# Kernel tuning notes

Hardware: AMD Instinct MI355X
Metric: run time of the kernel (lower is better)

Reference implementation:

```python
import math
import jax, jax.numpy as jnp
import numpy as np

B, N, DQ, DK, DV, H = 8, 1024, 256, 256, 256, 8
EPS_SM = 1e-15
EPS_LN = 1e-5


def _layer_norm(x, g, b):
    mu = jnp.mean(x, axis=-1, keepdims=True)
    var = jnp.mean((x - mu) ** 2, axis=-1, keepdims=True)
    return (x - mu) * jax.lax.rsqrt(var + EPS_LN) * g + b


def setup_inputs() -> dict:
    key = jax.random.key(0)
    ks = jax.random.split(key, 16)
    s = 0.05
    inp = {
        "Q": jax.random.normal(ks[0], (B, N, DQ), jnp.float32),
        "K": jax.random.normal(ks[1], (B, N, DK), jnp.float32),
        "lengths": jnp.clip(jax.random.randint(ks[2], (B,), 0, N), 1, N),
        "Wq": jax.random.normal(ks[3], (DQ, DV), jnp.float32) * s,
        "bq": jnp.zeros((DV,), jnp.float32),
        "Wk": jax.random.normal(ks[4], (DK, DV), jnp.float32) * s,
        "bk": jnp.zeros((DV,), jnp.float32),
        "Wv": jax.random.normal(ks[5], (DK, DV), jnp.float32) * s,
        "bv": jnp.zeros((DV,), jnp.float32),
        "Wo": jax.random.normal(ks[6], (DV, DV), jnp.float32) * s,
        "bo": jnp.zeros((DV,), jnp.float32),
        "g0": jnp.ones((DV,), jnp.float32),
        "b0": jnp.zeros((DV,), jnp.float32),
        "g1": jnp.ones((DV,), jnp.float32),
        "b1": jnp.zeros((DV,), jnp.float32),
    }
    return inp


def reference(Q, K, lengths, Wq, bq, Wk, bk, Wv, bv, Wo, bo, g0, b0, g1, b1):
    d = DV // H  # head dim
    mask = (jnp.arange(N) < lengths[:, None]).astype(Q.dtype)  # (B, N)
    q = (Q @ Wq + bq) * mask[..., None]  # (B, N, DV)
    k = (K @ Wk + bk) * mask[..., None]
    v = (K @ Wv + bv) * mask[..., None]
    qh = q.reshape(B, N, H, d)
    kh = k.reshape(B, N, H, d)
    vh = v.reshape(B, N, H, d)
    # NB: original scales by sqrt(dim_V), not sqrt(head_dim)
    scores = jnp.einsum("bnhd,bmhd->bhnm", qh, kh) / math.sqrt(DV)
    # set_softmax: raw exp, mask rows and cols by lengths, normalize over keys
    e = jnp.exp(scores) * mask[:, None, :, None] * mask[:, None, None, :]
    A = e / (jnp.sum(e, axis=-1, keepdims=True) + EPS_SM)  # (B, H, N, N)
    O = qh + jnp.einsum("bhnm,bmhd->bnhd", A, vh)  # residual per head
    O = O.reshape(B, N, DV)
    O = _layer_norm(O, g0, b0)
    O = O + jax.nn.relu(O @ Wo + bo)
    O = _layer_norm(O, g1, b1)
    return O
```

## Files before the change

### kernel.cpp

```cpp
#include <hip/hip_runtime.h>
#include <hip/hip_bf16.h>


typedef __attribute__((ext_vector_type(8))) short short8;
typedef __attribute__((ext_vector_type(4))) short short4v;
typedef __attribute__((ext_vector_type(4))) float f32x4;

__device__ __forceinline__ short f2bf(float f) {
    union { float f; unsigned u; } x; x.f = f;
    unsigned r = x.u + 0x7fffu + ((x.u >> 16) & 1u);
    return (short)(r >> 16);
}
__device__ __forceinline__ float bf2f(short s) {
    union { unsigned u; float f; } x; x.u = ((unsigned)(unsigned short)s) << 16;
    return x.f;
}

__global__ __launch_bounds__(256) void wtrans_kernel(
    const float* __restrict__ Wq, const float* __restrict__ Wk,
    const float* __restrict__ Wv, const float* __restrict__ Wo,
    short* __restrict__ WqT, short* __restrict__ WkT,
    short* __restrict__ WvT, short* __restrict__ WoT)
{
    const float* W; short* T;
    switch (blockIdx.y) {
        case 0:  W = Wq; T = WqT; break;
        case 1:  W = Wk; T = WkT; break;
        case 2:  W = Wv; T = WvT; break;
        default: W = Wo; T = WoT; break;
    }
    int base = blockIdx.x * 4096 + threadIdx.x;
    #pragma unroll
    for (int i = 0; i < 16; i++) {
        int e = base + i * 256;
        int n = e >> 8, k = e & 255;
        T[e] = f2bf(W[k * 256 + n]);
    }
}

__global__ __launch_bounds__(256) void proj_kernel(
    const float* __restrict__ Q, const float* __restrict__ Kin,
    const short* __restrict__ WqT, const short* __restrict__ WkT, const short* __restrict__ WvT,
    const float* __restrict__ bq, const float* __restrict__ bk, const float* __restrict__ bv,
    const int* __restrict__ lengths,
    short* __restrict__ qb, short* __restrict__ kb, short* __restrict__ vT)
{
    const int which = blockIdx.y;
    const float* A    = (which == 0) ? Q   : Kin;
    const short* WT   = (which == 0) ? WqT : (which == 1) ? WkT : WvT;
    const float* bias = (which == 0) ? bq  : (which == 1) ? bk  : bv;

    const int tid = threadIdx.x;
    const int lane = tid & 63, wid = tid >> 6;
    const int m = lane & 15, quad = lane >> 4;
    const int rh = wid >> 1, ch = wid & 1;
    const int r0 = blockIdx.x * 32 + rh * 16;
    const int c0 = ch * 128;
    const int b = blockIdx.x >> 5;
    const int len = lengths[b];
    const int ntok0 = r0 & 1023;

    f32x4 acc[8];
    #pragma unroll
    for (int t = 0; t < 8; t++) acc[t] = (f32x4){0.f, 0.f, 0.f, 0.f};

    if (ntok0 < len) {
        const float* arow = A + (size_t)(r0 + m) * 256;
        for (int kk = 0; kk < 256; kk += 32) {
            const float* ap = arow + kk + quad * 8;
            float4 f0 = *(const float4*)(ap);
            float4 f1 = *(const float4*)(ap + 4);
            short8 af;
            af[0] = f2bf(f0.x); af[1] = f2bf(f0.y); af[2] = f2bf(f0.z); af[3] = f2bf(f0.w);
            af[4] = f2bf(f1.x); af[5] = f2bf(f1.y); af[6] = f2bf(f1.z); af[7] = f2bf(f1.w);
            #pragma unroll
            for (int t = 0; t < 8; t++) {
                short8 bf = *(const short8*)(WT + (c0 + t * 16 + m) * 256 + kk + quad * 8);
                acc[t] = __builtin_amdgcn_mfma_f32_16x16x32_bf16(af, bf, acc[t], 0, 0, 0);
            }
        }
    }

    #pragma unroll
    for (int t = 0; t < 8; t++) {
        int n = c0 + t * 16 + m;
        float bv_ = bias[n];
        int h = n >> 5, i = n & 31;
        int bh = b * 8 + h;
        #pragma unroll
        for (int reg = 0; reg < 4; reg++) {
            int ntok = ntok0 + quad * 4 + reg;
            float val = (ntok < len) ? (acc[t][reg] + bv_) : 0.f;
            short s = f2bf(val);
            if (which == 2) {
                vT[(size_t)(bh * 32 + i) * 1024 + ntok] = s;
            } else {
                short* dst = (which == 0) ? qb : kb;
                dst[((size_t)bh * 1024 + ntok) * 32 + i] = s;
            }
        }
    }
}

__global__ __launch_bounds__(256) void attn_kernel(
    const short* __restrict__ qb, const short* __restrict__ kb, const short* __restrict__ vT,
    const int* __restrict__ lengths, float* __restrict__ O1)
{
    __shared__ short P[4][16][72];
    __shared__ float cbO[2][16][33];
    __shared__ float cbL[2][16];
    const int tid = threadIdx.x;
    const int lane = tid & 63, wid = tid >> 6;
    const int m = lane & 15, quad = lane >> 4;
    const int ks = wid & 1, qh = wid >> 1;
    const int bh = blockIdx.y;
    const int b = bh >> 3, h = bh & 7;
    const int len = lengths[b];
    const int qr0 = blockIdx.x * 32 + qh * 16;

    const short* qbase = qb + (size_t)bh * 1024 * 32;
    const short* kbase = kb + (size_t)bh * 1024 * 32;
    const short* vbase = vT + (size_t)bh * 32 * 1024;

    const short8 qf = *(const short8*)(qbase + (qr0 + m) * 32 + quad * 8);

    f32x4 o0 = (f32x4){0.f, 0.f, 0.f, 0.f};
    f32x4 o1 = (f32x4){0.f, 0.f, 0.f, 0.f};
    float l[4] = {0.f, 0.f, 0.f, 0.f};

    const int kbeg = ks * 512;
    int kchunks = 0;
    if (qr0 < len && len > kbeg) {
        int rem = len - kbeg;
        kchunks = rem >= 512 ? 8 : ((rem + 63) >> 6);
    }

    for (int ci = 0; ci < kchunks; ci++) {
        int key0 = kbeg + ci * 64;
        #pragma unroll
        for (int t = 0; t < 4; t++) {
            short8 kf = *(const short8*)(kbase + (key0 + t * 16 + m) * 32 + quad * 8);
            f32x4 s = __builtin_amdgcn_mfma_f32_16x16x32_bf16(qf, kf,
                        (f32x4){0.f, 0.f, 0.f, 0.f}, 0, 0, 0);
            int col = key0 + t * 16 + m;
            bool cm = col < len;
            #pragma unroll
            for (int reg = 0; reg < 4; reg++) {
                float e = cm ? __expf(s[reg] * 0.0625f) : 0.f;
                l[reg] += e;
                P[wid][quad * 4 + reg][t * 16 + m] = f2bf(e);
            }
        }
        asm volatile("s_waitcnt lgkmcnt(0)" ::: "memory");
        #pragma unroll
        for (int c = 0; c < 2; c++) {
            short8 pf  = *(const short8*)(&P[wid][m][c * 32 + quad * 8]);
            short8 vf0 = *(const short8*)(vbase + (size_t)(m) * 1024      + key0 + c * 32 + quad * 8);
            short8 vf1 = *(const short8*)(vbase + (size_t)(16 + m) * 1024 + key0 + c * 32 + quad * 8);
            o0 = __builtin_amdgcn_mfma_f32_16x16x32_bf16(pf, vf0, o0, 0, 0, 0);
            o1 = __builtin_amdgcn_mfma_f32_16x16x32_bf16(pf, vf1, o1, 0, 0, 0);
        }
    }

    #pragma unroll
    for (int reg = 0; reg < 4; reg++) {
        float s = l[reg];
        s += __shfl_xor(s, 1); s += __shfl_xor(s, 2);
        s += __shfl_xor(s, 4); s += __shfl_xor(s, 8);
        l[reg] = s;
    }

    if (ks == 1) {
        #pragma unroll
        for (int reg = 0; reg < 4; reg++) {
            cbO[qh][quad * 4 + reg][m]      = o0[reg];
            cbO[qh][quad * 4 + reg][16 + m] = o1[reg];
        }
        if (m == 0) {
            #pragma unroll
            for (int reg = 0; reg < 4; reg++) cbL[qh][quad * 4 + reg] = l[reg];
        }
    }
    __syncthreads();
    if (ks == 0) {
        const int hbase = h * 32;
        #pragma unroll
        for (int reg = 0; reg < 4; reg++) {
            int r = quad * 4 + reg;
            o0[reg] += cbO[qh][r][m];
            o1[reg] += cbO[qh][r][16 + m];
            float lt = l[reg] + cbL[qh][r];
            int qrow = qr0 + r;
            float f = (qrow < len) ? 1.f / (lt + 1e-15f) : 0.f;
            size_t obase = ((size_t)(b * 1024 + qrow)) * 256 + hbase;
            float q0 = bf2f(qbase[qrow * 32 + m]);
            float q1 = bf2f(qbase[qrow * 32 + 16 + m]);
            O1[obase + m]      = q0 + o0[reg] * f;
            O1[obase + 16 + m] = q1 + o1[reg] * f;
        }
    }
}

__global__ __launch_bounds__(256) void ln0_kernel(
    const float* __restrict__ O1, const float* __restrict__ g0, const float* __restrict__ b0,
    short* __restrict__ Xb)
{
    const int tid = threadIdx.x;
    const int lane = tid & 63, wid = tid >> 6;
    const int token = blockIdx.x * 4 + wid;
    const float* row = O1 + (size_t)token * 256;
    float4 x = *(const float4*)(row + lane * 4);
    float s  = x.x + x.y + x.z + x.w;
    float s2 = x.x * x.x + x.y * x.y + x.z * x.z + x.w * x.w;
    #pragma unroll
    for (int msk = 1; msk < 64; msk <<= 1) {
        s  += __shfl_xor(s, msk);
        s2 += __shfl_xor(s2, msk);
    }
    float mean = s * (1.f / 256.f);
    float var  = s2 * (1.f / 256.f) - mean * mean;
    float rs = rsqrtf(var + 1e-5f);
    float4 g = *(const float4*)(g0 + lane * 4);
    float4 bb = *(const float4*)(b0 + lane * 4);
    short4v y;
    y[0] = f2bf((x.x - mean) * rs * g.x + bb.x);
    y[1] = f2bf((x.y - mean) * rs * g.y + bb.y);
    y[2] = f2bf((x.z - mean) * rs * g.z + bb.z);
    y[3] = f2bf((x.w - mean) * rs * g.w + bb.w);
    *(short4v*)(Xb + (size_t)token * 256 + lane * 4) = y;
}

__global__ __launch_bounds__(256) void out_kernel(
    const short* __restrict__ Xb, const short* __restrict__ WoT,
    const float* __restrict__ bo, const float* __restrict__ g1, const float* __restrict__ b1,
    float* __restrict__ out)
{
    __shared__ float st[2][2][2][16];
    const int tid = threadIdx.x;
    const int lane = tid & 63, wid = tid >> 6;
    const int m = lane & 15, quad = lane >> 4;
    const int rh = wid >> 1, ch = wid & 1;
    const int r0 = blockIdx.x * 32 + rh * 16;
    const int c0 = ch * 128;

    f32x4 acc[8];
    #pragma unroll
    for (int t = 0; t < 8; t++) acc[t] = (f32x4){0.f, 0.f, 0.f, 0.f};

    const short* arow = Xb + (size_t)(r0 + m) * 256;
    for (int kk = 0; kk < 256; kk += 32) {
        short8 af = *(const short8*)(arow + kk + quad * 8);
        #pragma unroll
        for (int t = 0; t < 8; t++) {
            short8 bf = *(const short8*)(WoT + (c0 + t * 16 + m) * 256 + kk + quad * 8);
            acc[t] = __builtin_amdgcn_mfma_f32_16x16x32_bf16(af, bf, acc[t], 0, 0, 0);
        }
    }

    float s1[4] = {0.f, 0.f, 0.f, 0.f};
    float s2[4] = {0.f, 0.f, 0.f, 0.f};
    #pragma unroll
    for (int t = 0; t < 8; t++) {
        int n = c0 + t * 16 + m;
        float bon = bo[n];
        #pragma unroll
        for (int reg = 0; reg < 4; reg++) {
            int token = r0 + quad * 4 + reg;
            float xv = bf2f(Xb[(size_t)token * 256 + n]);
            float c = acc[t][reg] + bon;
            float yv = xv + (c > 0.f ? c : 0.f);
            acc[t][reg] = yv;
            s1[reg] += yv;
            s2[reg] += yv * yv;
        }
    }
    #pragma unroll
    for (int reg = 0; reg < 4; reg++) {
        float a = s1[reg], bsum = s2[reg];
        a += __shfl_xor(a, 1); a += __shfl_xor(a, 2); a += __shfl_xor(a, 4); a += __shfl_xor(a, 8);
        bsum += __shfl_xor(bsum, 1); bsum += __shfl_xor(bsum, 2); bsum += __shfl_xor(bsum, 4); bsum += __shfl_xor(bsum, 8);
        s1[reg] = a; s2[reg] = bsum;
    }
    if (m == 0) {
        #pragma unroll
        for (int reg = 0; reg < 4; reg++) {
            st[rh][ch][0][quad * 4 + reg] = s1[reg];
            st[rh][ch][1][quad * 4 + reg] = s2[reg];
        }
    }
    __syncthreads();
    #pragma unroll
    for (int reg = 0; reg < 4; reg++) {
        int r = quad * 4 + reg;
        float t1 = s1[reg] + st[rh][ch ^ 1][0][r];
        float t2 = s2[reg] + st[rh][ch ^ 1][1][r];
        float mean = t1 * (1.f / 256.f);
        float var  = t2 * (1.f / 256.f) - mean * mean;
        float rs = rsqrtf(var + 1e-5f);
        int token = r0 + r;
        #pragma unroll
        for (int t = 0; t < 8; t++) {
            int n = c0 + t * 16 + m;
            out[(size_t)token * 256 + n] = (acc[t][reg] - mean) * rs * g1[n] + b1[n];
        }
    }
}

extern "C" void kernel_launch(void* const* d_in, const int* in_sizes, int n_in,
                              void* d_out, int out_size, void* d_ws, size_t ws_size,
                              hipStream_t stream) {
    const float* Q   = (const float*)d_in[0];
    const float* K   = (const float*)d_in[1];
    const int* lengths = (const int*)d_in[2];
    const float* Wq  = (const float*)d_in[3];
    const float* bq  = (const float*)d_in[4];
    const float* Wk  = (const float*)d_in[5];
    const float* bk  = (const float*)d_in[6];
    const float* Wv  = (const float*)d_in[7];
    const float* bv  = (const float*)d_in[8];
    const float* Wo  = (const float*)d_in[9];
    const float* bo  = (const float*)d_in[10];
    const float* g0  = (const float*)d_in[11];
    const float* b0  = (const float*)d_in[12];
    const float* g1  = (const float*)d_in[13];
    const float* b1  = (const float*)d_in[14];
    float* out = (float*)d_out;

    char* ws = (char*)d_ws;
    short* qb  = (short*)(ws);
    short* kb  = (short*)(ws + (4u << 20));
    short* vT  = (short*)(ws + (8u << 20));
    float* O1  = (float*)(ws + (12u << 20));
    short* Xb  = (short*)(ws + (20u << 20));
    short* WqT = (short*)(ws + (24u << 20));
    short* WkT = (short*)(ws + (24u << 20) + (128u << 10));
    short* WvT = (short*)(ws + (24u << 20) + (256u << 10));
    short* WoT = (short*)(ws + (24u << 20) + (384u << 10));

    wtrans_kernel<<<dim3(16, 4), 256, 0, stream>>>(Wq, Wk, Wv, Wo, WqT, WkT, WvT, WoT);
    proj_kernel<<<dim3(256, 3), 256, 0, stream>>>(Q, K, WqT, WkT, WvT, bq, bk, bv,
                                                  lengths, qb, kb, vT);
    attn_kernel<<<dim3(32, 64), 256, 0, stream>>>(qb, kb, vT, lengths, O1);
    ln0_kernel<<<dim3(2048), 256, 0, stream>>>(O1, g0, b0, Xb);
    out_kernel<<<dim3(256), 256, 0, stream>>>(Xb, WoT, bo, g1, b1, out);
}
```

Baseline: 166.2 us.

## Restructure attention blocks to cover all heads for a 16-row query tile

Each attention block now handles 16 query rows across all 8 heads, one wave per head, and walks every key chunk itself instead of splitting keys across two waves and merging partial sums through shared memory. This removes the cross-wave reduction and its shared buffers. In exchange it adds block-wide barriers around each key chunk, halves the key-level parallelism per query tile and makes each wave process up to twice as many chunks serially. The barriers are unnecessary because each wave only touches its own P slice.

```diff
diff --git a/kernel.cpp b/kernel.cpp
--- a/kernel.cpp
+++ b/kernel.cpp
@@ -102,21 +102,18 @@
     }
 }
 
-__global__ __launch_bounds__(256) void attn_kernel(
+__global__ __launch_bounds__(512) void attn_kernel(
     const short* __restrict__ qb, const short* __restrict__ kb, const short* __restrict__ vT,
     const int* __restrict__ lengths, float* __restrict__ O1)
 {
-    __shared__ short P[4][16][72];
-    __shared__ float cbO[2][16][33];
-    __shared__ float cbL[2][16];
+    __shared__ short P[8][16][72];
     const int tid = threadIdx.x;
-    const int lane = tid & 63, wid = tid >> 6;
+    const int lane = tid & 63, h = tid >> 6;
     const int m = lane & 15, quad = lane >> 4;
-    const int ks = wid & 1, qh = wid >> 1;
-    const int bh = blockIdx.y;
-    const int b = bh >> 3, h = bh & 7;
+    const int b = blockIdx.y;
     const int len = lengths[b];
-    const int qr0 = blockIdx.x * 32 + qh * 16;
+    const int qr0 = blockIdx.x * 16;
+    const int bh = b * 8 + h;
 
     const short* qbase = qb + (size_t)bh * 1024 * 32;
     const short* kbase = kb + (size_t)bh * 1024 * 32;
@@ -128,15 +125,10 @@
     f32x4 o1 = (f32x4){0.f, 0.f, 0.f, 0.f};
     float l[4] = {0.f, 0.f, 0.f, 0.f};
 
-    const int kbeg = ks * 512;
-    int kchunks = 0;
-    if (qr0 < len && len > kbeg) {
-        int rem = len - kbeg;
-        kchunks = rem >= 512 ? 8 : ((rem + 63) >> 6);
-    }
+    const int kchunks = (qr0 < len) ? ((len + 63) >> 6) : 0;
 
     for (int ci = 0; ci < kchunks; ci++) {
-        int key0 = kbeg + ci * 64;
+        int key0 = ci * 64;
         #pragma unroll
         for (int t = 0; t < 4; t++) {
             short8 kf = *(const short8*)(kbase + (key0 + t * 16 + m) * 32 + quad * 8);
@@ -148,18 +140,19 @@
             for (int reg = 0; reg < 4; reg++) {
                 float e = cm ? __expf(s[reg] * 0.0625f) : 0.f;
                 l[reg] += e;
-                P[wid][quad * 4 + reg][t * 16 + m] = f2bf(e);
+                P[h][quad * 4 + reg][t * 16 + m] = f2bf(e);
             }
         }
-        asm volatile("s_waitcnt lgkmcnt(0)" ::: "memory");
+        __syncthreads();
         #pragma unroll
         for (int c = 0; c < 2; c++) {
-            short8 pf  = *(const short8*)(&P[wid][m][c * 32 + quad * 8]);
+            short8 pf  = *(const short8*)(&P[h][m][c * 32 + quad * 8]);
             short8 vf0 = *(const short8*)(vbase + (size_t)(m) * 1024      + key0 + c * 32 + quad * 8);
             short8 vf1 = *(const short8*)(vbase + (size_t)(16 + m) * 1024 + key0 + c * 32 + quad * 8);
             o0 = __builtin_amdgcn_mfma_f32_16x16x32_bf16(pf, vf0, o0, 0, 0, 0);
             o1 = __builtin_amdgcn_mfma_f32_16x16x32_bf16(pf, vf1, o1, 0, 0, 0);
         }
+        __syncthreads();
     }
 
     #pragma unroll
@@ -170,34 +163,17 @@
         l[reg] = s;
     }
 
-    if (ks == 1) {
-        #pragma unroll
-        for (int reg = 0; reg < 4; reg++) {
-            cbO[qh][quad * 4 + reg][m]      = o0[reg];
-            cbO[qh][quad * 4 + reg][16 + m] = o1[reg];
-        }
-        if (m == 0) {
-            #pragma unroll
-            for (int reg = 0; reg < 4; reg++) cbL[qh][quad * 4 + reg] = l[reg];
-        }
-    }
-    __syncthreads();
-    if (ks == 0) {
-        const int hbase = h * 32;
-        #pragma unroll
-        for (int reg = 0; reg < 4; reg++) {
-            int r = quad * 4 + reg;
-            o0[reg] += cbO[qh][r][m];
-            o1[reg] += cbO[qh][r][16 + m];
-            float lt = l[reg] + cbL[qh][r];
-            int qrow = qr0 + r;
-            float f = (qrow < len) ? 1.f / (lt + 1e-15f) : 0.f;
-            size_t obase = ((size_t)(b * 1024 + qrow)) * 256 + hbase;
-            float q0 = bf2f(qbase[qrow * 32 + m]);
-            float q1 = bf2f(qbase[qrow * 32 + 16 + m]);
-            O1[obase + m]      = q0 + o0[reg] * f;
-            O1[obase + 16 + m] = q1 + o1[reg] * f;
-        }
+    const int hbase = h * 32;
+    #pragma unroll
+    for (int reg = 0; reg < 4; reg++) {
+        int r = quad * 4 + reg;
+        int qrow = qr0 + r;
+        float f = (qrow < len) ? 1.f / (l[reg] + 1e-15f) : 0.f;
+        size_t obase = ((size_t)(b * 1024 + qrow)) * 256 + hbase;
+        float q0 = bf2f(qbase[qrow * 32 + m]);
+        float q1 = bf2f(qbase[qrow * 32 + 16 + m]);
+        O1[obase + m]      = q0 + o0[reg] * f;
+        O1[obase + 16 + m] = q1 + o1[reg] * f;
     }
 }
 
@@ -340,7 +316,7 @@
     wtrans_kernel<<<dim3(16, 4), 256, 0, stream>>>(Wq, Wk, Wv, Wo, WqT, WkT, WvT, WoT);
     proj_kernel<<<dim3(256, 3), 256, 0, stream>>>(Q, K, WqT, WkT, WvT, bq, bk, bv,
                                                   lengths, qb, kb, vT);
-    attn_kernel<<<dim3(32, 64), 256, 0, stream>>>(qb, kb, vT, lengths, O1);
+    attn_kernel<<<dim3(64, 8), 512, 0, stream>>>(qb, kb, vT, lengths, O1);
     ln0_kernel<<<dim3(2048), 256, 0, stream>>>(O1, g0, b0, Xb);
     out_kernel<<<dim3(256), 256, 0, stream>>>(Xb, WoT, bo, g1, b1, out);
 }
```

Result: slower. 181.2 us (+9.1%).
